# Performance work log

Hardware: AMD Instinct MI355X
Metric: run time of the kernel (lower is better)

Reference implementation:

```python
import jax, jax.numpy as jnp
import numpy as np

H = 200
W = 200
SH = 2.0  # h / h_meters = 200/100
SW = 2.0
THRESH = 0.05   # opacity prune threshold
CHUNK = 128     # gaussians per scan step
EPS_T = 1e-4    # 3DGS transmittance early-stop
ALPHA_MIN = 1.0 / 255.0


def _rasterize(means3D, colors, opac, cov3D):
    """Orthographic BEV 3D-Gaussian-splat rasterization for one sample.
    means3D (N,3), colors (N,d), opac (N,1), cov3D (N,6) packed [xx,xy,xz,yy,yz,zz].
    Returns (d, H, W) image. Depth is identically 0 under the BEV view matrix,
    so compositing order is the input order (stable), matching the CUDA sort.
    """
    N, d = colors.shape
    P = H * W
    # pixel centers, row-major flatten: p = y*W + x
    gy, gx = jnp.meshgrid(jnp.arange(H, dtype=jnp.float32),
                          jnp.arange(W, dtype=jnp.float32), indexing='ij')
    pxf = gx.reshape(-1)
    pyf = gy.reshape(-1)

    # project means with full_proj_transform: u = -sh*y + H/2, v = -sw*x + W/2
    u = -SH * means3D[:, 1] + H / 2.0
    v = -SW * means3D[:, 0] + W / 2.0

    # 2D covariance: W2 @ Cov3D @ W2^T + 0.3*I with W2 = [[0,sh,0],[sw,0,0]]
    a = SH * SH * cov3D[:, 3] + 0.3   # var along image x (from Sigma_yy)
    c = SW * SW * cov3D[:, 0] + 0.3   # var along image y (from Sigma_xx)
    b = SH * SW * cov3D[:, 1]
    det = a * c - b * b
    valid = det > 0.0
    det_s = jnp.where(valid, det, 1.0)
    conA = c / det_s
    conB = b / det_s   # power uses +conB*dx*dy (conic.y = -b/det in CUDA)
    conC = a / det_s

    # fold pruning mask (opacity threshold) and validity into opacity
    op = jnp.where((opac[:, 0] > THRESH) & valid, opac[:, 0], 0.0)

    K = N // CHUNK
    chunks = tuple(t.reshape(K, CHUNK, *t.shape[1:])
                   for t in (u, v, conA, conB, conC, op, colors))

    def body(carry, ch):
        img, T = carry  # img (P,d), T (P,)
        u_, v_, A_, B_, C_, op_, col_ = ch
        dx = u_[:, None] - pxf[None, :]          # (C,P)
        dy = v_[:, None] - pyf[None, :]
        power = -0.5 * (A_[:, None] * dx * dx + C_[:, None] * dy * dy) \
                + B_[:, None] * dx * dy
        alpha = jnp.minimum(0.99, op_[:, None] * jnp.exp(jnp.minimum(power, 0.0)))
        # CUDA skips power>0 and alpha < 1/255
        alpha = jnp.where((power > 0.0) | (alpha < ALPHA_MIN), 0.0, alpha)
        # early termination: skip gaussian i (and all after) once T would drop < 1e-4
        T_incl = T[None, :] * jnp.cumprod(1.0 - alpha, axis=0)
        alpha = jnp.where(T_incl < EPS_T, 0.0, alpha)
        cp = jnp.cumprod(1.0 - alpha, axis=0)    # inclusive products
        T_excl = jnp.concatenate([jnp.ones((1, P), dtype=cp.dtype), cp[:-1]], axis=0)
        wgt = alpha * T_excl * T[None, :]        # (C,P)
        img = img + jnp.einsum('cp,cd->pd', wgt, col_)
        T = T * cp[-1]
        return (img, T), None

    img0 = jnp.zeros((P, d), dtype=colors.dtype)
    T0 = jnp.ones((P,), dtype=colors.dtype)
    (img, T), _ = jax.lax.scan(body, (img0, T0), chunks)
    # background is zeros -> no bg term; reshape to (d, H, W)
    return img.reshape(H, W, d).transpose(2, 0, 1)


def setup_inputs() -> dict:
    key = jax.random.key(0)
    k1, k2, k3, k4 = jax.random.split(key, 4)
    B, N, D = 2, 1024, 32
    features = jax.random.normal(k1, (B, N, D), dtype=jnp.float32)
    # BEV covers +/-50m; scale positions so most gaussians land on the canvas
    means3D = jax.random.normal(k2, (B, N, 3), dtype=jnp.float32) * 20.0
    cov3D = jax.random.uniform(k3, (B, N, 6), dtype=jnp.float32)
    opacities = jax.random.uniform(k4, (B, N, 1), dtype=jnp.float32)
    return {"features": features, "means3D": means3D,
            "cov3D": cov3D, "opacities": opacities}


def reference(features, means3D, cov3D, opacities):
    bev = jax.vmap(_rasterize)(means3D, features, opacities, cov3D)  # (B,d,H,W)
    mask = opacities[..., 0] > THRESH
    mean_count = mask.astype(jnp.float32).sum(axis=1).mean()
    return bev, mean_count
```

## Files before the change

### kernel.cpp

```cpp
#include <hip/hip_runtime.h>


#define HH 200
#define WW 200
#define DD 32
#define NG 1024
#define BB 2
#define OUT_IMG (BB*DD*HH*WW)
#define NW 4
#define SEGG (NG/NW)
#define NGRP (SEGG/64)

__device__ __forceinline__ float rlane(float x, int l) {
    return __uint_as_float(__builtin_amdgcn_readlane(__float_as_uint(x), l));
}

__global__ __launch_bounds__(64*NW, 4) void render_kernel(
    const float* __restrict__ feats,
    const float* __restrict__ means,
    const float* __restrict__ cov,
    const float* __restrict__ opac,
    float* __restrict__ out)
{
    __shared__ float4 simg[NW][64][8];
    __shared__ float sT[NW][64];
    __shared__ float wsum[NW];

    const int b    = blockIdx.z;
    const int tid  = threadIdx.x;
    const int lane = tid & 63;
    const int wid  = tid >> 6;
    const int px   = blockIdx.x*8 + (lane & 7);
    const int py   = blockIdx.y*8 + (lane >> 3);
    const float pxf = (float)px, pyf = (float)py;
    const float cx  = blockIdx.x*8 + 3.5f;
    const float cy  = blockIdx.y*8 + 3.5f;

    const float* __restrict__ featsB = feats + (size_t)b * NG * DD;
    const int gB = b * NG;

    float4 acc[8];
#pragma unroll
    for (int j = 0; j < 8; ++j) acc[j] = make_float4(0.f,0.f,0.f,0.f);
    float T = 1.f, P = 1.f;
    bool skip = false;

    for (int k = 0; k < NGRP; ++k) {
        const int gbase = wid*SEGG + k*64;
        const int g  = gB + gbase + lane;
        const float o   = opac[g];
        const float2 c01 = *(const float2*)(cov + (size_t)g*6);
        const float c3  = cov[(size_t)g*6 + 3];
        const float av = 4.f*c3    + 0.3f;
        const float cv = 4.f*c01.x + 0.3f;
        const float bv = 4.f*c01.y;
        const float det = av*cv - bv*bv;
        bool flag = false;
        float u=0.f, v=0.f, A=0.f, Bc=0.f, Cc=0.f, pl=0.f;
        if (o > 0.05f && det > 0.f) {
            u = -2.f*means[(size_t)g*3+1] + 100.f;
            v = -2.f*means[(size_t)g*3+0] + 100.f;
            pl = -__logf(255.f*o);
            const float qmax = -2.f*pl;
            const float htr = 0.5f*(av+cv), hdf = 0.5f*(av-cv);
            const float lmax = htr + sqrtf(hdf*hdf + bv*bv);
            const float r = sqrtf(qmax*lmax) + 0.5f;
            if (fabsf(u - cx) <= 3.5f + r && fabsf(v - cy) <= 3.5f + r) {
                const float inv = 1.f/det;
                A = cv*inv; Bc = bv*inv; Cc = av*inv;
                flag = true;
            }
        }
        unsigned long long mm = __ballot(flag);
        if (!skip) {
            while (mm) {
                const int i = (int)__builtin_ctzll(mm);
                mm &= mm - 1ull;
                const float ui  = rlane(u,  i);
                const float vi  = rlane(v,  i);
                const float Ai  = rlane(A,  i);
                const float Bi  = rlane(Bc, i);
                const float Ci  = rlane(Cc, i);
                const float oi  = rlane(o,  i);
                const float pli = rlane(pl, i);
                const float dx = ui - pxf;
                const float dy = vi - pyf;
                const float pw = fmaf(Bi, dx*dy, -0.5f*(Ai*dx*dx + Ci*dy*dy));
                if (pw > 0.f) continue;
                if (pw < pli - 1e-3f) continue;
                const float alpha = fminf(0.99f, oi * __expf(pw));
                if (alpha < (1.f/255.f)) continue;
                const float om = 1.f - alpha;
                const float tp = T * P;
                if (tp * om < 1e-4f) { skip = true; break; }
                const float w = alpha * tp;
                const float4* __restrict__ col =
                    (const float4*)(featsB + (size_t)(gbase + i) * DD);
#pragma unroll
                for (int j = 0; j < 8; ++j) {
                    const float4 c4 = col[j];
                    acc[j].x = fmaf(w, c4.x, acc[j].x);
                    acc[j].y = fmaf(w, c4.y, acc[j].y);
                    acc[j].z = fmaf(w, c4.z, acc[j].z);
                    acc[j].w = fmaf(w, c4.w, acc[j].w);
                }
                P *= om;
            }
        }
        if (k & 1) { T *= P; P = 1.f; skip = false; }
    }

    sT[wid][lane] = T * P;
#pragma unroll
    for (int j = 0; j < 8; ++j)
        simg[wid][lane][(j + lane) & 7] = acc[j];
    __syncthreads();

    {
        const int p   = tid & 63;
        const int grp = tid >> 6;
        const float t0 = sT[0][p], t1 = sT[1][p], t2 = sT[2][p];
        const float pf1 = t0, pf2 = t0*t1, pf3 = pf2*t2;
        const int ppx = blockIdx.x*8 + (p & 7);
        const int ppy = blockIdx.y*8 + (p >> 3);
        const size_t base = (size_t)b * DD * (HH*WW) + (size_t)ppy * WW + ppx;
#pragma unroll
        for (int q = 0; q < 2; ++q) {
            const int c4 = grp*2 + q;
            const int slot = (c4 + p) & 7;
            const float4 r0 = simg[0][p][slot];
            const float4 r1 = simg[1][p][slot];
            const float4 r2 = simg[2][p][slot];
            const float4 r3 = simg[3][p][slot];
            float4 ov;
            ov.x = fmaf(pf3, r3.x, fmaf(pf2, r2.x, fmaf(pf1, r1.x, r0.x)));
            ov.y = fmaf(pf3, r3.y, fmaf(pf2, r2.y, fmaf(pf1, r1.y, r0.y)));
            ov.z = fmaf(pf3, r3.z, fmaf(pf2, r2.z, fmaf(pf1, r1.z, r0.z)));
            ov.w = fmaf(pf3, r3.w, fmaf(pf2, r2.w, fmaf(pf1, r1.w, r0.w)));
            out[base + (size_t)(c4*4+0)*(HH*WW)] = ov.x;
            out[base + (size_t)(c4*4+1)*(HH*WW)] = ov.y;
            out[base + (size_t)(c4*4+2)*(HH*WW)] = ov.z;
            out[base + (size_t)(c4*4+3)*(HH*WW)] = ov.w;
        }
    }

    if (blockIdx.x == 0 && blockIdx.y == 0 && b == 0) {
        float s = 0.f;
        for (int i = tid; i < BB*NG; i += 64*NW)
            s += (opac[i] > 0.05f) ? 1.f : 0.f;
#pragma unroll
        for (int off = 32; off > 0; off >>= 1)
            s += __shfl_down(s, off, 64);
        if (lane == 0) wsum[wid] = s;
        __syncthreads();
        if (tid == 0)
            out[OUT_IMG] = (wsum[0]+wsum[1]+wsum[2]+wsum[3]) * (1.f/(float)BB);
    }
}

extern "C" void kernel_launch(void* const* d_in, const int* in_sizes, int n_in,
                              void* d_out, int out_size, void* d_ws, size_t ws_size,
                              hipStream_t stream) {
    const float* feats = (const float*)d_in[0];
    const float* means = (const float*)d_in[1];
    const float* cvr   = (const float*)d_in[2];
    const float* opc   = (const float*)d_in[3];
    float* out = (float*)d_out;

    render_kernel<<<dim3(WW/8, HH/8, BB), dim3(64*NW), 0, stream>>>(
        feats, means, cvr, opc, out);
}
```

Baseline: 72.76 us.

## Precompute and compact visible gaussians in a prep kernel before rendering

Adds a small prep kernel that computes each gaussian's projected centre, conic, radius and opacity once per batch. It writes only the gaussians that survive the opacity, determinant and canvas-overlap tests into a stable, order-preserving compacted workspace list, and records the count. The render kernel then reads this packed list and splits it evenly across its four waves, instead of recomputing the logs, square roots and divides in every tile and scanning all gaussians. The mean-count output now comes from the prep kernel's count. The cost is an extra kernel launch and a serialising dependency through global memory.

```diff
diff --git a/kernel.cpp b/kernel.cpp
--- a/kernel.cpp
+++ b/kernel.cpp
@@ -8,47 +8,35 @@
 #define BB 2
 #define OUT_IMG (BB*DD*HH*WW)
 #define NW 4
-#define SEGG (NG/NW)
-#define NGRP (SEGG/64)
+#define WS_ENT4(b,e) ((((b)<<10) + (e)) << 1)
+#define WS_INT_OFF 16384
 
 __device__ __forceinline__ float rlane(float x, int l) {
     return __uint_as_float(__builtin_amdgcn_readlane(__float_as_uint(x), l));
 }
 
-__global__ __launch_bounds__(64*NW, 4) void render_kernel(
-    const float* __restrict__ feats,
+__global__ __launch_bounds__(256) void prep_kernel(
     const float* __restrict__ means,
     const float* __restrict__ cov,
     const float* __restrict__ opac,
-    float* __restrict__ out)
+    float* __restrict__ ws)
 {
-    __shared__ float4 simg[NW][64][8];
-    __shared__ float sT[NW][64];
-    __shared__ float wsum[NW];
-
-    const int b    = blockIdx.z;
+    const int b    = blockIdx.x;
     const int tid  = threadIdx.x;
     const int lane = tid & 63;
     const int wid  = tid >> 6;
-    const int px   = blockIdx.x*8 + (lane & 7);
-    const int py   = blockIdx.y*8 + (lane >> 3);
-    const float pxf = (float)px, pyf = (float)py;
-    const float cx  = blockIdx.x*8 + 3.5f;
-    const float cy  = blockIdx.y*8 + 3.5f;
-
-    const float* __restrict__ featsB = feats + (size_t)b * NG * DD;
-    const int gB = b * NG;
-
-    float4 acc[8];
-#pragma unroll
-    for (int j = 0; j < 8; ++j) acc[j] = make_float4(0.f,0.f,0.f,0.f);
-    float T = 1.f, P = 1.f;
-    bool skip = false;
-
-    for (int k = 0; k < NGRP; ++k) {
-        const int gbase = wid*SEGG + k*64;
-        const int g  = gB + gbase + lane;
+    __shared__ int wcnt[NW];
+    float4* __restrict__ ws4 = (float4*)ws;
+    int*    __restrict__ wsi = (int*)ws;
+
+    int base = 0;
+    int opc  = 0;
+
+    for (int r = 0; r < NG/256; ++r) {
+        const int gl = r*256 + tid;
+        const int g  = b*NG + gl;
         const float o   = opac[g];
+        opc += (o > 0.05f) ? 1 : 0;
         const float2 c01 = *(const float2*)(cov + (size_t)g*6);
         const float c3  = cov[(size_t)g*6 + 3];
         const float av = 4.f*c3    + 0.3f;
@@ -56,61 +44,120 @@
         const float bv = 4.f*c01.y;
         const float det = av*cv - bv*bv;
         bool flag = false;
-        float u=0.f, v=0.f, A=0.f, Bc=0.f, Cc=0.f, pl=0.f;
+        float4 q0 = make_float4(0.f,0.f,0.f,0.f);
+        float4 q1 = make_float4(0.f,0.f,0.f,0.f);
         if (o > 0.05f && det > 0.f) {
-            u = -2.f*means[(size_t)g*3+1] + 100.f;
-            v = -2.f*means[(size_t)g*3+0] + 100.f;
-            pl = -__logf(255.f*o);
-            const float qmax = -2.f*pl;
+            const float u = -2.f*means[(size_t)g*3+1] + 100.f;
+            const float v = -2.f*means[(size_t)g*3+0] + 100.f;
+            const float qmax = 2.f*__logf(255.f*o);
             const float htr = 0.5f*(av+cv), hdf = 0.5f*(av-cv);
             const float lmax = htr + sqrtf(hdf*hdf + bv*bv);
-            const float r = sqrtf(qmax*lmax) + 0.5f;
-            if (fabsf(u - cx) <= 3.5f + r && fabsf(v - cy) <= 3.5f + r) {
+            const float rr = sqrtf(qmax*lmax) + 0.5f;
+            if (fabsf(u - 99.5f) <= 99.51f + rr &&
+                fabsf(v - 99.5f) <= 99.51f + rr) {
                 const float inv = 1.f/det;
-                A = cv*inv; Bc = bv*inv; Cc = av*inv;
+                q0 = make_float4(u, v, cv*inv, bv*inv);
+                q1 = make_float4(av*inv, rr, o, __int_as_float(gl));
                 flag = true;
             }
         }
+        const unsigned long long mask = __ballot(flag);
+        if (lane == 0) wcnt[wid] = (int)__popcll(mask);
+        __syncthreads();
+        const int pre = (wid>0 ? wcnt[0]:0) + (wid>1 ? wcnt[1]:0)
+                      + (wid>2 ? wcnt[2]:0);
+        if (flag) {
+            const int e = base + pre +
+                (int)__popcll(mask & ((1ull << lane) - 1ull));
+            ws4[WS_ENT4(b,e)    ] = q0;
+            ws4[WS_ENT4(b,e) + 1] = q1;
+        }
+        base += wcnt[0]+wcnt[1]+wcnt[2]+wcnt[3];
+        __syncthreads();
+    }
+
+#pragma unroll
+    for (int off = 32; off > 0; off >>= 1) opc += __shfl_down(opc, off, 64);
+    if (lane == 0) wcnt[wid] = opc;
+    __syncthreads();
+    if (tid == 0) {
+        wsi[WS_INT_OFF + b]     = base;
+        wsi[WS_INT_OFF + 2 + b] = wcnt[0]+wcnt[1]+wcnt[2]+wcnt[3];
+    }
+}
+
+__global__ __launch_bounds__(64*NW, 4) void render_kernel(
+    const float* __restrict__ feats,
+    const float* __restrict__ ws,
+    float* __restrict__ out)
+{
+    __shared__ float4 simg[NW][64][8];
+    __shared__ float sT[NW][64];
+
+    const int b    = blockIdx.z;
+    const int tid  = threadIdx.x;
+    const int lane = tid & 63;
+    const int wid  = tid >> 6;
+    const float pxf = (float)(blockIdx.x*8 + (lane & 7));
+    const float pyf = (float)(blockIdx.y*8 + (lane >> 3));
+    const float cx  = blockIdx.x*8 + 3.5f;
+    const float cy  = blockIdx.y*8 + 3.5f;
+
+    const float4* __restrict__ ws4 = (const float4*)ws;
+    const int*    __restrict__ wsi = (const int*)ws;
+    const float*  __restrict__ featsB = feats + (size_t)b * NG * DD;
+
+    const int cnt = wsi[WS_INT_OFF + b];
+    const int Q   = (cnt + 3) >> 2;
+    const int e0w = wid * Q;
+    const int e1w = min(e0w + Q, cnt);
+
+    float4 acc[8];
+#pragma unroll
+    for (int j = 0; j < 8; ++j) acc[j] = make_float4(0.f,0.f,0.f,0.f);
+    float T = 1.f;
+    bool alive = true;
+
+    for (int e0 = e0w; e0 < e1w && alive; e0 += 64) {
+        const int e = e0 + lane;
+        const float4 q0 = ws4[WS_ENT4(b,e)    ];
+        const float4 q1 = ws4[WS_ENT4(b,e) + 1];
+        const bool flag = (e < e1w) &&
+            fabsf(q0.x - cx) <= 3.5f + q1.y &&
+            fabsf(q0.y - cy) <= 3.5f + q1.y;
         unsigned long long mm = __ballot(flag);
-        if (!skip) {
-            while (mm) {
-                const int i = (int)__builtin_ctzll(mm);
-                mm &= mm - 1ull;
-                const float ui  = rlane(u,  i);
-                const float vi  = rlane(v,  i);
-                const float Ai  = rlane(A,  i);
-                const float Bi  = rlane(Bc, i);
-                const float Ci  = rlane(Cc, i);
-                const float oi  = rlane(o,  i);
-                const float pli = rlane(pl, i);
-                const float dx = ui - pxf;
-                const float dy = vi - pyf;
-                const float pw = fmaf(Bi, dx*dy, -0.5f*(Ai*dx*dx + Ci*dy*dy));
-                if (pw > 0.f) continue;
-                if (pw < pli - 1e-3f) continue;
-                const float alpha = fminf(0.99f, oi * __expf(pw));
-                if (alpha < (1.f/255.f)) continue;
-                const float om = 1.f - alpha;
-                const float tp = T * P;
-                if (tp * om < 1e-4f) { skip = true; break; }
-                const float w = alpha * tp;
-                const float4* __restrict__ col =
-                    (const float4*)(featsB + (size_t)(gbase + i) * DD);
-#pragma unroll
-                for (int j = 0; j < 8; ++j) {
-                    const float4 c4 = col[j];
-                    acc[j].x = fmaf(w, c4.x, acc[j].x);
-                    acc[j].y = fmaf(w, c4.y, acc[j].y);
-                    acc[j].z = fmaf(w, c4.z, acc[j].z);
-                    acc[j].w = fmaf(w, c4.w, acc[j].w);
-                }
-                P *= om;
+        while (mm) {
+            const int i = (int)__builtin_ctzll(mm);
+            mm &= mm - 1ull;
+            const float dx = rlane(q0.x, i) - pxf;
+            const float dy = rlane(q0.y, i) - pyf;
+            const float Ai = rlane(q0.z, i);
+            const float Bi = rlane(q0.w, i);
+            const float Ci = rlane(q1.x, i);
+            const float pw = fmaf(Bi, dx*dy, -0.5f*(Ai*dx*dx + Ci*dy*dy));
+            if (pw > 0.f) continue;
+            const float oi = rlane(q1.z, i);
+            const float alpha = fminf(0.99f, oi * __expf(pw));
+            if (alpha < (1.f/255.f)) continue;
+            const float om = 1.f - alpha;
+            if (T * om < 1e-4f) { alive = false; break; }
+            const float w = alpha * T;
+            const int gi = __builtin_amdgcn_readlane(__float_as_int(q1.w), i);
+            const float4* __restrict__ col =
+                (const float4*)(featsB + (size_t)gi * DD);
+#pragma unroll
+            for (int j = 0; j < 8; ++j) {
+                const float4 c4 = col[j];
+                acc[j].x = fmaf(w, c4.x, acc[j].x);
+                acc[j].y = fmaf(w, c4.y, acc[j].y);
+                acc[j].z = fmaf(w, c4.z, acc[j].z);
+                acc[j].w = fmaf(w, c4.w, acc[j].w);
             }
-        }
-        if (k & 1) { T *= P; P = 1.f; skip = false; }
-    }
-
-    sT[wid][lane] = T * P;
+            T *= om;
+        }
+    }
+
+    sT[wid][lane] = T;
 #pragma unroll
     for (int j = 0; j < 8; ++j)
         simg[wid][lane][(j + lane) & 7] = acc[j];
@@ -144,18 +191,8 @@
         }
     }
 
-    if (blockIdx.x == 0 && blockIdx.y == 0 && b == 0) {
-        float s = 0.f;
-        for (int i = tid; i < BB*NG; i += 64*NW)
-            s += (opac[i] > 0.05f) ? 1.f : 0.f;
-#pragma unroll
-        for (int off = 32; off > 0; off >>= 1)
-            s += __shfl_down(s, off, 64);
-        if (lane == 0) wsum[wid] = s;
-        __syncthreads();
-        if (tid == 0)
-            out[OUT_IMG] = (wsum[0]+wsum[1]+wsum[2]+wsum[3]) * (1.f/(float)BB);
-    }
+    if (blockIdx.x == 0 && blockIdx.y == 0 && b == 0 && tid == 0)
+        out[OUT_IMG] = (float)(wsi[WS_INT_OFF+2] + wsi[WS_INT_OFF+3]) * 0.5f;
 }
 
 extern "C" void kernel_launch(void* const* d_in, const int* in_sizes, int n_in,
@@ -166,7 +203,9 @@
     const float* cvr   = (const float*)d_in[2];
     const float* opc   = (const float*)d_in[3];
     float* out = (float*)d_out;
-
+    float* ws  = (float*)d_ws;
+
+    prep_kernel<<<dim3(BB), dim3(256), 0, stream>>>(means, cvr, opc, ws);
     render_kernel<<<dim3(WW/8, HH/8, BB), dim3(64*NW), 0, stream>>>(
-        feats, means, cvr, opc, out);
-}
+        feats, ws, out);
+}
```

New measurement: 76.05 us. 1.05x slower.

## Render 64-pixel row strips per wave with LDS-staged gaussian preprocessing

Applied to the files above, without the earlier changes.

Each block now preprocesses all 1024 gaussians of its batch into shared memory: projected centre, conic, cull radius and opacity. Each wave then composites one 64-pixel row strip over all gaussians in order, culling them against the strip. This removes the per-tile recomputation of gaussian parameters and the cross-wave transmittance merge through shared memory, and makes the output stores coalesced along rows. In exchange the grid shrinks to 200 blocks of 512 threads, each wave walks the whole gaussian list serially, and the wider strips let more gaussians pass the cull test, which risks lower GPU occupancy and longer serial chains.

```diff
diff --git a/kernel.cpp b/kernel.cpp
--- a/kernel.cpp
+++ b/kernel.cpp
@@ -7,154 +7,138 @@
 #define NG 1024
 #define BB 2
 #define OUT_IMG (BB*DD*HH*WW)
-#define NW 4
-#define SEGG (NG/NW)
-#define NGRP (SEGG/64)
+#define ALPHA_MIN (1.0f/255.0f)
 
 __device__ __forceinline__ float rlane(float x, int l) {
     return __uint_as_float(__builtin_amdgcn_readlane(__float_as_uint(x), l));
 }
 
-__global__ __launch_bounds__(64*NW, 4) void render_kernel(
+__global__ __launch_bounds__(512) void render_kernel(
     const float* __restrict__ feats,
     const float* __restrict__ means,
     const float* __restrict__ cov,
     const float* __restrict__ opac,
     float* __restrict__ out)
 {
-    __shared__ float4 simg[NW][64][8];
-    __shared__ float sT[NW][64];
-    __shared__ float wsum[NW];
+    __shared__ float su[NG], sv[NG], sr[NG], sA[NG], sB[NG], sC[NG], sO[NG];
+    __shared__ int csum[8];
 
     const int b    = blockIdx.z;
     const int tid  = threadIdx.x;
     const int lane = tid & 63;
     const int wid  = tid >> 6;
-    const int px   = blockIdx.x*8 + (lane & 7);
-    const int py   = blockIdx.y*8 + (lane >> 3);
-    const float pxf = (float)px, pyf = (float)py;
-    const float cx  = blockIdx.x*8 + 3.5f;
-    const float cy  = blockIdx.y*8 + 3.5f;
 
-    const float* __restrict__ featsB = feats + (size_t)b * NG * DD;
-    const int gB = b * NG;
+    for (int r0 = 0; r0 < NG; r0 += 512) {
+        const int gl = r0 + tid;
+        const int g  = b*NG + gl;
+        const float o   = opac[g];
+        const float2 c01 = *(const float2*)(cov + (size_t)g*6);
+        const float c3  = cov[(size_t)g*6 + 3];
+        const float m0  = means[(size_t)g*3 + 0];
+        const float m1  = means[(size_t)g*3 + 1];
+        const float av = 4.f*c3    + 0.3f;
+        const float cv = 4.f*c01.x + 0.3f;
+        const float bv = 4.f*c01.y;
+        const float det = av*cv - bv*bv;
+        float u=0.f, v=0.f, rr=-1e30f, A=0.f, Bc=0.f, Cc=0.f;
+        if (o > 0.05f && det > 0.f) {
+            u = -2.f*m1 + 100.f;
+            v = -2.f*m0 + 100.f;
+            const float qmax = 2.f*__logf(255.f*o);
+            const float htr = 0.5f*(av+cv), hdf = 0.5f*(av-cv);
+            const float lmax = htr + sqrtf(hdf*hdf + bv*bv);
+            rr = sqrtf(qmax*lmax) + 0.5f;
+            const float inv = 1.f/det;
+            A = cv*inv; Bc = bv*inv; Cc = av*inv;
+        }
+        su[gl]=u; sv[gl]=v; sr[gl]=rr; sA[gl]=A; sB[gl]=Bc; sC[gl]=Cc; sO[gl]=o;
+    }
+
+    if (blockIdx.x == 0 && b == 0) {
+        int s = 0;
+        for (int i = tid; i < BB*NG; i += 512)
+            s += (opac[i] > 0.05f) ? 1 : 0;
+#pragma unroll
+        for (int off = 32; off; off >>= 1) s += __shfl_down(s, off, 64);
+        if (lane == 0) csum[wid] = s;
+    }
+    __syncthreads();
+    if (blockIdx.x == 0 && b == 0 && tid == 0) {
+        int t = 0;
+#pragma unroll
+        for (int wq = 0; wq < 8; ++wq) t += csum[wq];
+        out[OUT_IMG] = (float)t * 0.5f;
+    }
+
+    const int S   = blockIdx.x*8 + wid;
+    const int y   = S >> 2;
+    const int sid = S & 3;
+    const int x0  = (sid < 3) ? sid*64 : 136;
+    const float pxf = (float)(x0 + lane);
+    const float pyf = (float)y;
+    const float cxf = x0 + 31.5f;
 
     float4 acc[8];
 #pragma unroll
     for (int j = 0; j < 8; ++j) acc[j] = make_float4(0.f,0.f,0.f,0.f);
-    float T = 1.f, P = 1.f;
-    bool skip = false;
+    float T = 1.f;
+    bool alive = true;
+    const float* __restrict__ featsB = feats + (size_t)b * NG * DD;
 
-    for (int k = 0; k < NGRP; ++k) {
-        const int gbase = wid*SEGG + k*64;
-        const int g  = gB + gbase + lane;
-        const float o   = opac[g];
-        const float2 c01 = *(const float2*)(cov + (size_t)g*6);
-        const float c3  = cov[(size_t)g*6 + 3];
-        const float av = 4.f*c3    + 0.3f;
-        const float cv = 4.f*c01.x + 0.3f;
-        const float bv = 4.f*c01.y;
-        const float det = av*cv - bv*bv;
-        bool flag = false;
-        float u=0.f, v=0.f, A=0.f, Bc=0.f, Cc=0.f, pl=0.f;
-        if (o > 0.05f && det > 0.f) {
-            u = -2.f*means[(size_t)g*3+1] + 100.f;
-            v = -2.f*means[(size_t)g*3+0] + 100.f;
-            pl = -__logf(255.f*o);
-            const float qmax = -2.f*pl;
-            const float htr = 0.5f*(av+cv), hdf = 0.5f*(av-cv);
-            const float lmax = htr + sqrtf(hdf*hdf + bv*bv);
-            const float r = sqrtf(qmax*lmax) + 0.5f;
-            if (fabsf(u - cx) <= 3.5f + r && fabsf(v - cy) <= 3.5f + r) {
-                const float inv = 1.f/det;
-                A = cv*inv; Bc = bv*inv; Cc = av*inv;
-                flag = true;
+    for (int e0 = 0; e0 < NG; e0 += 64) {
+        if (__ballot(alive) == 0ull) break;
+        const int e = e0 + lane;
+        const float ru = su[e], rv = sv[e], rr = sr[e];
+        const float rA = sA[e], rB = sB[e], rC = sC[e], rO = sO[e];
+        const bool flag = (fabsf(ru - cxf) <= 31.5f + rr) &&
+                          (fabsf(rv - pyf) <= rr);
+        unsigned long long mm = __ballot(flag);
+        while (mm) {
+            const int i = (int)__builtin_ctzll(mm);
+            mm &= mm - 1ull;
+            const int gi = e0 + i;
+            const float4* __restrict__ col =
+                (const float4*)(featsB + (size_t)gi * DD);
+            const float4 f0=col[0], f1=col[1], f2=col[2], f3=col[3],
+                         f4=col[4], f5=col[5], f6=col[6], f7=col[7];
+            const float dx = rlane(ru, i) - pxf;
+            const float dy = rlane(rv, i) - pyf;
+            const float pw = fmaf(rlane(rB, i), dx*dy,
+                              -0.5f*(rlane(rA, i)*dx*dx + rlane(rC, i)*dy*dy));
+            const float alpha = fminf(0.99f, rlane(rO, i) * __expf(pw));
+            const float om = 1.f - alpha;
+            bool ok = alive && (pw <= 0.f) && (alpha >= ALPHA_MIN);
+            if (ok && (T*om < 1e-4f)) { alive = false; ok = false; }
+            if (ok) {
+                const float w = alpha * T;
+                acc[0].x=fmaf(w,f0.x,acc[0].x); acc[0].y=fmaf(w,f0.y,acc[0].y);
+                acc[0].z=fmaf(w,f0.z,acc[0].z); acc[0].w=fmaf(w,f0.w,acc[0].w);
+                acc[1].x=fmaf(w,f1.x,acc[1].x); acc[1].y=fmaf(w,f1.y,acc[1].y);
+                acc[1].z=fmaf(w,f1.z,acc[1].z); acc[1].w=fmaf(w,f1.w,acc[1].w);
+                acc[2].x=fmaf(w,f2.x,acc[2].x); acc[2].y=fmaf(w,f2.y,acc[2].y);
+                acc[2].z=fmaf(w,f2.z,acc[2].z); acc[2].w=fmaf(w,f2.w,acc[2].w);
+                acc[3].x=fmaf(w,f3.x,acc[3].x); acc[3].y=fmaf(w,f3.y,acc[3].y);
+                acc[3].z=fmaf(w,f3.z,acc[3].z); acc[3].w=fmaf(w,f3.w,acc[3].w);
+                acc[4].x=fmaf(w,f4.x,acc[4].x); acc[4].y=fmaf(w,f4.y,acc[4].y);
+                acc[4].z=fmaf(w,f4.z,acc[4].z); acc[4].w=fmaf(w,f4.w,acc[4].w);
+                acc[5].x=fmaf(w,f5.x,acc[5].x); acc[5].y=fmaf(w,f5.y,acc[5].y);
+                acc[5].z=fmaf(w,f5.z,acc[5].z); acc[5].w=fmaf(w,f5.w,acc[5].w);
+                acc[6].x=fmaf(w,f6.x,acc[6].x); acc[6].y=fmaf(w,f6.y,acc[6].y);
+                acc[6].z=fmaf(w,f6.z,acc[6].z); acc[6].w=fmaf(w,f6.w,acc[6].w);
+                acc[7].x=fmaf(w,f7.x,acc[7].x); acc[7].y=fmaf(w,f7.y,acc[7].y);
+                acc[7].z=fmaf(w,f7.z,acc[7].z); acc[7].w=fmaf(w,f7.w,acc[7].w);
+                T *= om;
             }
-        }
-        unsigned long long mm = __ballot(flag);
-        if (!skip) {
-            while (mm) {
-                const int i = (int)__builtin_ctzll(mm);
-                mm &= mm - 1ull;
-                const float ui  = rlane(u,  i);
-                const float vi  = rlane(v,  i);
-                const float Ai  = rlane(A,  i);
-                const float Bi  = rlane(Bc, i);
-                const float Ci  = rlane(Cc, i);
-                const float oi  = rlane(o,  i);
-                const float pli = rlane(pl, i);
-                const float dx = ui - pxf;
-                const float dy = vi - pyf;
-                const float pw = fmaf(Bi, dx*dy, -0.5f*(Ai*dx*dx + Ci*dy*dy));
-                if (pw > 0.f) continue;
-                if (pw < pli - 1e-3f) continue;
-                const float alpha = fminf(0.99f, oi * __expf(pw));
-                if (alpha < (1.f/255.f)) continue;
-                const float om = 1.f - alpha;
-                const float tp = T * P;
-                if (tp * om < 1e-4f) { skip = true; break; }
-                const float w = alpha * tp;
-                const float4* __restrict__ col =
-                    (const float4*)(featsB + (size_t)(gbase + i) * DD);
-#pragma unroll
-                for (int j = 0; j < 8; ++j) {
-                    const float4 c4 = col[j];
-                    acc[j].x = fmaf(w, c4.x, acc[j].x);
-                    acc[j].y = fmaf(w, c4.y, acc[j].y);
-                    acc[j].z = fmaf(w, c4.z, acc[j].z);
-                    acc[j].w = fmaf(w, c4.w, acc[j].w);
-                }
-                P *= om;
-            }
-        }
-        if (k & 1) { T *= P; P = 1.f; skip = false; }
-    }
-
-    sT[wid][lane] = T * P;
-#pragma unroll
-    for (int j = 0; j < 8; ++j)
-        simg[wid][lane][(j + lane) & 7] = acc[j];
-    __syncthreads();
-
-    {
-        const int p   = tid & 63;
-        const int grp = tid >> 6;
-        const float t0 = sT[0][p], t1 = sT[1][p], t2 = sT[2][p];
-        const float pf1 = t0, pf2 = t0*t1, pf3 = pf2*t2;
-        const int ppx = blockIdx.x*8 + (p & 7);
-        const int ppy = blockIdx.y*8 + (p >> 3);
-        const size_t base = (size_t)b * DD * (HH*WW) + (size_t)ppy * WW + ppx;
-#pragma unroll
-        for (int q = 0; q < 2; ++q) {
-            const int c4 = grp*2 + q;
-            const int slot = (c4 + p) & 7;
-            const float4 r0 = simg[0][p][slot];
-            const float4 r1 = simg[1][p][slot];
-            const float4 r2 = simg[2][p][slot];
-            const float4 r3 = simg[3][p][slot];
-            float4 ov;
-            ov.x = fmaf(pf3, r3.x, fmaf(pf2, r2.x, fmaf(pf1, r1.x, r0.x)));
-            ov.y = fmaf(pf3, r3.y, fmaf(pf2, r2.y, fmaf(pf1, r1.y, r0.y)));
-            ov.z = fmaf(pf3, r3.z, fmaf(pf2, r2.z, fmaf(pf1, r1.z, r0.z)));
-            ov.w = fmaf(pf3, r3.w, fmaf(pf2, r2.w, fmaf(pf1, r1.w, r0.w)));
-            out[base + (size_t)(c4*4+0)*(HH*WW)] = ov.x;
-            out[base + (size_t)(c4*4+1)*(HH*WW)] = ov.y;
-            out[base + (size_t)(c4*4+2)*(HH*WW)] = ov.z;
-            out[base + (size_t)(c4*4+3)*(HH*WW)] = ov.w;
         }
     }
 
-    if (blockIdx.x == 0 && blockIdx.y == 0 && b == 0) {
-        float s = 0.f;
-        for (int i = tid; i < BB*NG; i += 64*NW)
-            s += (opac[i] > 0.05f) ? 1.f : 0.f;
+    const size_t base = (size_t)b * DD * (HH*WW) + (size_t)y * WW + x0 + lane;
 #pragma unroll
-        for (int off = 32; off > 0; off >>= 1)
-            s += __shfl_down(s, off, 64);
-        if (lane == 0) wsum[wid] = s;
-        __syncthreads();
-        if (tid == 0)
-            out[OUT_IMG] = (wsum[0]+wsum[1]+wsum[2]+wsum[3]) * (1.f/(float)BB);
+    for (int j = 0; j < 8; ++j) {
+        out[base + (size_t)(4*j+0)*(HH*WW)] = acc[j].x;
+        out[base + (size_t)(4*j+1)*(HH*WW)] = acc[j].y;
+        out[base + (size_t)(4*j+2)*(HH*WW)] = acc[j].z;
+        out[base + (size_t)(4*j+3)*(HH*WW)] = acc[j].w;
     }
 }
 
@@ -167,6 +151,6 @@
     const float* opc   = (const float*)d_in[3];
     float* out = (float*)d_out;
 
-    render_kernel<<<dim3(WW/8, HH/8, BB), dim3(64*NW), 0, stream>>>(
+    render_kernel<<<dim3(100, 1, BB), dim3(512), 0, stream>>>(
         feats, means, cvr, opc, out);
 }
```

Measured after the change: 81.89 us. +12.6%, slower.

## Process two tiles per block reusing per-gaussian preprocessing in registers

Applied to the files above, without the earlier changes.

Each block now handles two horizontally spaced 8x8 tiles, computing projected means, conics and cull radii once into registers and reusing them for both tiles. The tile-overlap test is rewritten as a squared-distance comparison to avoid a sqrt per tile. This halves the grid size, which reduces redundant setup work but lowers parallelism and serialises blending work inside each block, and it increases register pressure from the per-group arrays.

```diff
diff --git a/kernel.cpp b/kernel.cpp
--- a/kernel.cpp
+++ b/kernel.cpp
@@ -10,6 +10,8 @@
 #define NW 4
 #define SEGG (NG/NW)
 #define NGRP (SEGG/64)
+#define TILES_X 25
+#define GRID_X 13
 
 __device__ __forceinline__ float rlane(float x, int l) {
     return __uint_as_float(__builtin_amdgcn_readlane(__float_as_uint(x), l));
@@ -30,118 +32,39 @@
     const int tid  = threadIdx.x;
     const int lane = tid & 63;
     const int wid  = tid >> 6;
-    const int px   = blockIdx.x*8 + (lane & 7);
-    const int py   = blockIdx.y*8 + (lane >> 3);
-    const float pxf = (float)px, pyf = (float)py;
-    const float cx  = blockIdx.x*8 + 3.5f;
+    const float pyf = (float)(blockIdx.y*8 + (lane >> 3));
     const float cy  = blockIdx.y*8 + 3.5f;
 
     const float* __restrict__ featsB = feats + (size_t)b * NG * DD;
     const int gB = b * NG;
 
-    float4 acc[8];
+    float u_[NGRP], v_[NGRP], A_[NGRP], B_[NGRP], C_[NGRP],
+          pl_[NGRP], o_[NGRP], q_[NGRP];
 #pragma unroll
-    for (int j = 0; j < 8; ++j) acc[j] = make_float4(0.f,0.f,0.f,0.f);
-    float T = 1.f, P = 1.f;
-    bool skip = false;
-
     for (int k = 0; k < NGRP; ++k) {
-        const int gbase = wid*SEGG + k*64;
-        const int g  = gB + gbase + lane;
+        const int g = gB + wid*SEGG + k*64 + lane;
         const float o   = opac[g];
         const float2 c01 = *(const float2*)(cov + (size_t)g*6);
         const float c3  = cov[(size_t)g*6 + 3];
+        const float m0  = means[(size_t)g*3 + 0];
+        const float m1  = means[(size_t)g*3 + 1];
         const float av = 4.f*c3    + 0.3f;
         const float cv = 4.f*c01.x + 0.3f;
         const float bv = 4.f*c01.y;
         const float det = av*cv - bv*bv;
-        bool flag = false;
-        float u=0.f, v=0.f, A=0.f, Bc=0.f, Cc=0.f, pl=0.f;
+        float u=1e30f, v=1e30f, A=0.f, Bc=0.f, Cc=0.f, pl=0.f, qlm=0.f;
         if (o > 0.05f && det > 0.f) {
-            u = -2.f*means[(size_t)g*3+1] + 100.f;
-            v = -2.f*means[(size_t)g*3+0] + 100.f;
+            u = -2.f*m1 + 100.f;
+            v = -2.f*m0 + 100.f;
             pl = -__logf(255.f*o);
-            const float qmax = -2.f*pl;
             const float htr = 0.5f*(av+cv), hdf = 0.5f*(av-cv);
             const float lmax = htr + sqrtf(hdf*hdf + bv*bv);
-            const float r = sqrtf(qmax*lmax) + 0.5f;
-            if (fabsf(u - cx) <= 3.5f + r && fabsf(v - cy) <= 3.5f + r) {
-                const float inv = 1.f/det;
-                A = cv*inv; Bc = bv*inv; Cc = av*inv;
-                flag = true;
-            }
+            qlm = -2.f*pl*lmax;
+            const float inv = 1.f/det;
+            A = cv*inv; Bc = bv*inv; Cc = av*inv;
         }
-        unsigned long long mm = __ballot(flag);
-        if (!skip) {
-            while (mm) {
-                const int i = (int)__builtin_ctzll(mm);
-                mm &= mm - 1ull;
-                const float ui  = rlane(u,  i);
-                const float vi  = rlane(v,  i);
-                const float Ai  = rlane(A,  i);
-                const float Bi  = rlane(Bc, i);
-                const float Ci  = rlane(Cc, i);
-                const float oi  = rlane(o,  i);
-                const float pli = rlane(pl, i);
-                const float dx = ui - pxf;
-                const float dy = vi - pyf;
-                const float pw = fmaf(Bi, dx*dy, -0.5f*(Ai*dx*dx + Ci*dy*dy));
-                if (pw > 0.f) continue;
-                if (pw < pli - 1e-3f) continue;
-                const float alpha = fminf(0.99f, oi * __expf(pw));
-                if (alpha < (1.f/255.f)) continue;
-                const float om = 1.f - alpha;
-                const float tp = T * P;
-                if (tp * om < 1e-4f) { skip = true; break; }
-                const float w = alpha * tp;
-                const float4* __restrict__ col =
-                    (const float4*)(featsB + (size_t)(gbase + i) * DD);
-#pragma unroll
-                for (int j = 0; j < 8; ++j) {
-                    const float4 c4 = col[j];
-                    acc[j].x = fmaf(w, c4.x, acc[j].x);
-                    acc[j].y = fmaf(w, c4.y, acc[j].y);
-                    acc[j].z = fmaf(w, c4.z, acc[j].z);
-                    acc[j].w = fmaf(w, c4.w, acc[j].w);
-                }
-                P *= om;
-            }
-        }
-        if (k & 1) { T *= P; P = 1.f; skip = false; }
-    }
-
-    sT[wid][lane] = T * P;
-#pragma unroll
-    for (int j = 0; j < 8; ++j)
-        simg[wid][lane][(j + lane) & 7] = acc[j];
-    __syncthreads();
-
-    {
-        const int p   = tid & 63;
-        const int grp = tid >> 6;
-        const float t0 = sT[0][p], t1 = sT[1][p], t2 = sT[2][p];
-        const float pf1 = t0, pf2 = t0*t1, pf3 = pf2*t2;
-        const int ppx = blockIdx.x*8 + (p & 7);
-        const int ppy = blockIdx.y*8 + (p >> 3);
-        const size_t base = (size_t)b * DD * (HH*WW) + (size_t)ppy * WW + ppx;
-#pragma unroll
-        for (int q = 0; q < 2; ++q) {
-            const int c4 = grp*2 + q;
-            const int slot = (c4 + p) & 7;
-            const float4 r0 = simg[0][p][slot];
-            const float4 r1 = simg[1][p][slot];
-            const float4 r2 = simg[2][p][slot];
-            const float4 r3 = simg[3][p][slot];
-            float4 ov;
-            ov.x = fmaf(pf3, r3.x, fmaf(pf2, r2.x, fmaf(pf1, r1.x, r0.x)));
-            ov.y = fmaf(pf3, r3.y, fmaf(pf2, r2.y, fmaf(pf1, r1.y, r0.y)));
-            ov.z = fmaf(pf3, r3.z, fmaf(pf2, r2.z, fmaf(pf1, r1.z, r0.z)));
-            ov.w = fmaf(pf3, r3.w, fmaf(pf2, r2.w, fmaf(pf1, r1.w, r0.w)));
-            out[base + (size_t)(c4*4+0)*(HH*WW)] = ov.x;
-            out[base + (size_t)(c4*4+1)*(HH*WW)] = ov.y;
-            out[base + (size_t)(c4*4+2)*(HH*WW)] = ov.z;
-            out[base + (size_t)(c4*4+3)*(HH*WW)] = ov.w;
-        }
+        u_[k]=u; v_[k]=v; A_[k]=A; B_[k]=Bc; C_[k]=Cc;
+        pl_[k]=pl; o_[k]=o; q_[k]=qlm;
     }
 
     if (blockIdx.x == 0 && blockIdx.y == 0 && b == 0) {
@@ -156,6 +79,100 @@
         if (tid == 0)
             out[OUT_IMG] = (wsum[0]+wsum[1]+wsum[2]+wsum[3]) * (1.f/(float)BB);
     }
+
+    for (int t = 0; t < 2; ++t) {
+        const int tx = blockIdx.x + t*GRID_X;
+        if (tx >= TILES_X) break;
+        const float pxf = (float)(tx*8 + (lane & 7));
+        const float cx  = tx*8 + 3.5f;
+
+        float4 acc[8];
+#pragma unroll
+        for (int j = 0; j < 8; ++j) acc[j] = make_float4(0.f,0.f,0.f,0.f);
+        float T = 1.f, P = 1.f;
+        bool skip = false;
+
+#pragma unroll
+        for (int k = 0; k < NGRP; ++k) {
+            const int gbase = wid*SEGG + k*64;
+            const float dmx = fmaxf(fabsf(u_[k] - cx), fabsf(v_[k] - cy)) - 4.f;
+            const bool flag = (dmx <= 0.f) || (dmx*dmx <= q_[k]);
+            unsigned long long mm = __ballot(flag);
+            if (!skip) {
+                while (mm) {
+                    const int i = (int)__builtin_ctzll(mm);
+                    mm &= mm - 1ull;
+                    const float ui  = rlane(u_[k],  i);
+                    const float vi  = rlane(v_[k],  i);
+                    const float Ai  = rlane(A_[k],  i);
+                    const float Bi  = rlane(B_[k],  i);
+                    const float Ci  = rlane(C_[k],  i);
+                    const float oi  = rlane(o_[k],  i);
+                    const float pli = rlane(pl_[k], i);
+                    const float dx = ui - pxf;
+                    const float dy = vi - pyf;
+                    const float pw = fmaf(Bi, dx*dy,
+                                          -0.5f*(Ai*dx*dx + Ci*dy*dy));
+                    if (pw > 0.f) continue;
+                    if (pw < pli - 1e-3f) continue;
+                    const float alpha = fminf(0.99f, oi * __expf(pw));
+                    if (alpha < (1.f/255.f)) continue;
+                    const float om = 1.f - alpha;
+                    const float tp = T * P;
+                    if (tp * om < 1e-4f) { skip = true; break; }
+                    const float w = alpha * tp;
+                    const float4* __restrict__ col =
+                        (const float4*)(featsB + (size_t)(gbase + i) * DD);
+#pragma unroll
+                    for (int j = 0; j < 8; ++j) {
+                        const float4 c4 = col[j];
+                        acc[j].x = fmaf(w, c4.x, acc[j].x);
+                        acc[j].y = fmaf(w, c4.y, acc[j].y);
+                        acc[j].z = fmaf(w, c4.z, acc[j].z);
+                        acc[j].w = fmaf(w, c4.w, acc[j].w);
+                    }
+                    P *= om;
+                }
+            }
+            if (k & 1) { T *= P; P = 1.f; skip = false; }
+        }
+
+        if (t) __syncthreads();
+        sT[wid][lane] = T;
+#pragma unroll
+        for (int j = 0; j < 8; ++j)
+            simg[wid][lane][(j + lane) & 7] = acc[j];
+        __syncthreads();
+
+        {
+            const int p   = tid & 63;
+            const int grp = tid >> 6;
+            const float t0 = sT[0][p], t1 = sT[1][p], t2 = sT[2][p];
+            const float pf1 = t0, pf2 = t0*t1, pf3 = pf2*t2;
+            const int ppx = tx*8 + (p & 7);
+            const int ppy = blockIdx.y*8 + (p >> 3);
+            const size_t base = (size_t)b * DD * (HH*WW)
+                              + (size_t)ppy * WW + ppx;
+#pragma unroll
+            for (int q = 0; q < 2; ++q) {
+                const int c4 = grp*2 + q;
+                const int slot = (c4 + p) & 7;
+                const float4 r0 = simg[0][p][slot];
+                const float4 r1 = simg[1][p][slot];
+                const float4 r2 = simg[2][p][slot];
+                const float4 r3 = simg[3][p][slot];
+                float4 ov;
+                ov.x = fmaf(pf3, r3.x, fmaf(pf2, r2.x, fmaf(pf1, r1.x, r0.x)));
+                ov.y = fmaf(pf3, r3.y, fmaf(pf2, r2.y, fmaf(pf1, r1.y, r0.y)));
+                ov.z = fmaf(pf3, r3.z, fmaf(pf2, r2.z, fmaf(pf1, r1.z, r0.z)));
+                ov.w = fmaf(pf3, r3.w, fmaf(pf2, r2.w, fmaf(pf1, r1.w, r0.w)));
+                out[base + (size_t)(c4*4+0)*(HH*WW)] = ov.x;
+                out[base + (size_t)(c4*4+1)*(HH*WW)] = ov.y;
+                out[base + (size_t)(c4*4+2)*(HH*WW)] = ov.z;
+                out[base + (size_t)(c4*4+3)*(HH*WW)] = ov.w;
+            }
+        }
+    }
 }
 
 extern "C" void kernel_launch(void* const* d_in, const int* in_sizes, int n_in,
@@ -167,6 +184,6 @@
     const float* opc   = (const float*)d_in[3];
     float* out = (float*)d_out;
 
-    render_kernel<<<dim3(WW/8, HH/8, BB), dim3(64*NW), 0, stream>>>(
+    render_kernel<<<dim3(GRID_X, HH/8, BB), dim3(64*NW), 0, stream>>>(
         feats, means, cvr, opc, out);
 }
```

Result: no change. 72.44 us (-0.4%).
